# Kernel optimization log

Measured on AMD Instinct MI355X. Metric: run time of the kernel, lower is better.

The kernel has to match this reference:

```python
import jax, jax.numpy as jnp
import numpy as np

NUM_HEADS = 16
KEY_DIM = 1024
VALUE_DIM = 1024
OUTPUT_DIM = 1024
D_MODEL = 1024


def setup_inputs() -> dict:
    key = jax.random.key(0)
    ks = jax.random.split(key, 12)
    B, S = 2, 2048
    inp = {
        'V': jax.random.normal(ks[0], (B, S, D_MODEL), dtype=jnp.float32),
        'Q': jax.random.normal(ks[1], (B, S, D_MODEL), dtype=jnp.float32),
        'K': jax.random.normal(ks[2], (B, S, D_MODEL), dtype=jnp.float32),
        'mask': jnp.ones((B, S, 1), dtype=jnp.float32),
        'WQ': jax.random.normal(ks[3], (D_MODEL, KEY_DIM), dtype=jnp.float32) * (1.0 / np.sqrt(D_MODEL)),
        'bQ': jnp.zeros((KEY_DIM,), dtype=jnp.float32),
        'WK': jax.random.normal(ks[4], (D_MODEL, KEY_DIM), dtype=jnp.float32) * (1.0 / np.sqrt(D_MODEL)),
        'bK': jnp.zeros((KEY_DIM,), dtype=jnp.float32),
        'WV': jax.random.normal(ks[5], (D_MODEL, VALUE_DIM), dtype=jnp.float32) * (1.0 / np.sqrt(D_MODEL)),
        'bV': jnp.zeros((VALUE_DIM,), dtype=jnp.float32),
        'WO': jax.random.normal(ks[6], (VALUE_DIM, OUTPUT_DIM), dtype=jnp.float32) * (1.0 / np.sqrt(VALUE_DIM)),
        'bO': jnp.zeros((OUTPUT_DIM,), dtype=jnp.float32),
    }
    return inp


def _split_heads(x, H):
    # [B, S, H*Dh] -> [B, H, S, Dh]
    B, S, D = x.shape
    return x.reshape(B, S, H, D // H).transpose(0, 2, 1, 3)


def reference(V, Q, K, mask, WQ, bQ, WK, bK, WV, bV, WO, bO):
    H = NUM_HEADS
    B, S, _ = Q.shape
    q = _split_heads(Q @ WQ + bQ, H)            # [B,H,S,Dh]
    k = _split_heads(K @ WK + bK, H)            # [B,H,S,Dh]
    scores = jnp.einsum('bhqd,bhkd->bhqk', q, k) / jnp.sqrt(jnp.float32(KEY_DIM))
    # hard mask: cross_mask = mask @ mask^T, broadcast over heads
    cross = jnp.einsum('bqi,bki->bqk', mask, mask)[:, None]  # [B,1,S,S]
    scores = jnp.where(cross > 0, scores, -jnp.inf)
    w = jax.nn.softmax(scores, axis=-1)          # [B,H,S,S]
    v = _split_heads(V @ WV + bV, H)             # [B,H,S,Dh]
    ctx = jnp.einsum('bhqk,bhkd->bhqd', w, v)    # [B,H,S,Dh]
    ctx = ctx.transpose(0, 2, 1, 3).reshape(B, S, -1)  # [B,S,H*Dh]
    out = ctx @ WO + bO                          # [B,S,output_dim]
    return out * mask
```

## Files before the change

### kernel.cpp

```cpp
#include <hip/hip_runtime.h>

typedef unsigned int uint;
typedef unsigned short u16;
using bf8    = __attribute__((ext_vector_type(8))) short;
using f32x4  = __attribute__((ext_vector_type(4))) float;
using f32x16 = __attribute__((ext_vector_type(16))) float;
using u16x4  = __attribute__((ext_vector_type(4))) unsigned short;

__device__ __forceinline__ u16 f2b(float f) {
    uint u = __builtin_bit_cast(uint, f);
    u += 0x7FFFu + ((u >> 16) & 1u);
    return (u16)(u >> 16);
}

#define CVTPK(lo, hi_) ({ uint r_; asm("v_cvt_pk_bf16_f32 %0, %1, %2" : "=v"(r_) : "v"(lo), "v"(hi_)); r_; })
#define SWAP32(a, b)   asm("v_permlane32_swap_b32 %0, %1" : "+v"(a), "+v"(b))

__device__ __forceinline__ void gload16(const void* g, void* l) {
    __builtin_amdgcn_global_load_lds(
        (const __attribute__((address_space(1))) unsigned int*)g,
        (__attribute__((address_space(3))) unsigned int*)l, 16, 0, 0);
}

__device__ __forceinline__ bf8 mk_pb(float p0, float p1, float p2, float p3,
                                     float p4, float p5, float p6, float p7) {
    uint a0 = CVTPK(p0, p1), b0 = CVTPK(p4, p5);
    uint a1 = CVTPK(p2, p3), b1 = CVTPK(p6, p7);
    SWAP32(a0, b0);
    SWAP32(a1, b1);
    union { uint u[4]; bf8 v; } r;
    r.u[0] = a0; r.u[1] = a1; r.u[2] = b0; r.u[3] = b1;
    return r.v;
}

__global__ __launch_bounds__(256) void k_wt(
    const float* __restrict__ w0, const float* __restrict__ w1,
    const float* __restrict__ w2, const float* __restrict__ w3,
    u16* __restrict__ o0, u16* __restrict__ o1,
    u16* __restrict__ o2, u16* __restrict__ o3)
{
    const float* w; u16* o;
    switch (blockIdx.z) {
        case 0: w = w0; o = o0; break;
        case 1: w = w1; o = o1; break;
        case 2: w = w2; o = o2; break;
        default: w = w3; o = o3; break;
    }
    __shared__ float t[32][33];
    int n0 = blockIdx.x * 32, k0 = blockIdx.y * 32;
    int tr = threadIdx.x >> 5, tc = threadIdx.x & 31;
    for (int i = 0; i < 4; ++i) {
        int r = i * 8 + tr;
        t[r][tc] = w[(size_t)(k0 + r) * 1024 + n0 + tc];
    }
    __syncthreads();
    for (int i = 0; i < 4; ++i) {
        int r = i * 8 + tr;
        o[(size_t)(n0 + r) * 1024 + k0 + tc] = f2b(t[tc][r]);
    }
}

__global__ __launch_bounds__(256) void k_cvt(
    const float* __restrict__ s0, const float* __restrict__ s1, const float* __restrict__ s2,
    u16* __restrict__ d0, u16* __restrict__ d1, u16* __restrict__ d2)
{
    const float* s; u16* d;
    switch (blockIdx.z) {
        case 0: s = s0; d = d0; break;
        case 1: s = s1; d = d1; break;
        default: s = s2; d = d2; break;
    }
    size_t i = ((size_t)blockIdx.x * 256 + threadIdx.x) * 8;
    float4 a = *(const float4*)(s + i);
    float4 b = *(const float4*)(s + i + 4);
    uint4 o;
    o.x = CVTPK(a.x, a.y);
    o.y = CVTPK(a.z, a.w);
    o.z = CVTPK(b.x, b.y);
    o.w = CVTPK(b.z, b.w);
    *(uint4*)(d + i) = o;
}

#define GEMM_BODY(A_, Bt_)                                                          \
    __shared__ u16 lA[128 * 64];                                                    \
    __shared__ u16 lB[128 * 64];                                                    \
    int tid = threadIdx.x;                                                          \
    int lane = tid & 63, wv = tid >> 6;                                             \
    int wm = wv >> 1, wn = wv & 1;                                                  \
    int m0 = blockIdx.x * 128, n0 = blockIdx.y * 128;                               \
    int lr = lane & 15, lg = lane >> 4;                                             \
    int sRow = lane >> 3, sCol = (lane & 7) * 8;                                    \
    f32x4 acc[4][4] = {};                                                           \
    for (int k0 = 0; k0 < 1024; k0 += 64) {                                         \
        __syncthreads();                                                            \
        _Pragma("unroll")                                                           \
        for (int c = 0; c < 4; ++c) {                                               \
            int rb = c * 32 + wv * 8;                                               \
            gload16(&A_[(size_t)(m0 + rb + sRow) * 1024 + k0 + sCol],               \
                    &lA[rb * 64 + lane * 8]);                                       \
            gload16(&Bt_[(size_t)(n0 + rb + sRow) * 1024 + k0 + sCol],              \
                    &lB[rb * 64 + lane * 8]);                                       \
        }                                                                           \
        __syncthreads();                                                            \
        _Pragma("unroll")                                                           \
        for (int kk = 0; kk < 64; kk += 32) {                                       \
            bf8 af[4], bfr[4];                                                      \
            int ko = kk + lg * 8;                                                   \
            _Pragma("unroll")                                                       \
            for (int m = 0; m < 4; ++m) af[m]  = *(const bf8*)&lA[(wm * 64 + m * 16 + lr) * 64 + ko]; \
            _Pragma("unroll")                                                       \
            for (int n = 0; n < 4; ++n) bfr[n] = *(const bf8*)&lB[(wn * 64 + n * 16 + lr) * 64 + ko]; \
            _Pragma("unroll")                                                       \
            for (int m = 0; m < 4; ++m)                                             \
                _Pragma("unroll")                                                   \
                for (int n = 0; n < 4; ++n)                                         \
                    acc[m][n] = __builtin_amdgcn_mfma_f32_16x16x32_bf16(af[m], bfr[n], acc[m][n], 0, 0, 0); \
        }                                                                           \
    }

__global__ __launch_bounds__(256) void k_gemm_qkv(
    const u16* __restrict__ Xq, const u16* __restrict__ Xk, const u16* __restrict__ Xv,
    const u16* __restrict__ WtQ, const u16* __restrict__ WtK, const u16* __restrict__ WtV,
    const float* __restrict__ bQ, const float* __restrict__ bK, const float* __restrict__ bV,
    u16* __restrict__ qn, u16* __restrict__ kn, u16* __restrict__ vth, float qscale)
{
    const u16 *A, *Bt; const float* bias; u16* outp; int epi; float scale;
    switch (blockIdx.z) {
        case 0:  A = Xq; Bt = WtQ; bias = bQ; outp = qn;  epi = 0; scale = qscale; break;
        case 1:  A = Xk; Bt = WtK; bias = bK; outp = kn;  epi = 0; scale = 1.0f;   break;
        default: A = Xv; Bt = WtV; bias = bV; outp = vth; epi = 1; scale = 1.0f;   break;
    }
    GEMM_BODY(A, Bt)
    for (int m = 0; m < 4; ++m) {
        int Rb = m0 + wm * 64 + m * 16 + lg * 4;
        for (int n = 0; n < 4; ++n) {
            int C = n0 + wn * 64 + n * 16 + lr;
            float bv = bias[C];
            if (epi == 0) {
                for (int r = 0; r < 4; ++r)
                    outp[(size_t)(Rb + r) * 1024 + C] = f2b((acc[m][n][r] + bv) * scale);
            } else {
                int h = C >> 6, dh = C & 63;
                int b = Rb >> 11, s = Rb & 2047;
                u16x4 pk;
                for (int r = 0; r < 4; ++r) pk[r] = f2b(acc[m][n][r] + bv);
                *(u16x4*)&vth[((size_t)(b * 16 + h) * 64 + dh) * 2048 + s] = pk;
            }
        }
    }
}

__global__ __launch_bounds__(256) void k_gemm_out(
    const u16* __restrict__ Actx, const u16* __restrict__ WtO,
    const float* __restrict__ bias, const float* __restrict__ mask,
    float* __restrict__ outp)
{
    GEMM_BODY(Actx, WtO)
    for (int m = 0; m < 4; ++m) {
        int Rb = m0 + wm * 64 + m * 16 + lg * 4;
        for (int n = 0; n < 4; ++n) {
            int C = n0 + wn * 64 + n * 16 + lr;
            float bv = bias[C];
            for (int r = 0; r < 4; ++r) {
                int R = Rb + r;
                outp[(size_t)R * 1024 + C] = (acc[m][n][r] + bv) * mask[R];
            }
        }
    }
}

__global__ __launch_bounds__(256) void k_flash(
    const u16* __restrict__ qn, const u16* __restrict__ kn,
    const u16* __restrict__ vt, u16* __restrict__ ctx)
{
    __shared__ char lK[8192];
    __shared__ char lV[8192];
    const int S = 2048;
    int bh = blockIdx.y;
    int b = bh >> 4, h = bh & 15;
    int q0 = blockIdx.x * 128;
    int tid = threadIdx.x, lane = tid & 63, w = tid >> 6;
    int l31 = lane & 31, hi = lane >> 5;

    int qrow = q0 + w * 32 + l31;
    bf8 qf[4];
    const u16* qbase = &qn[((size_t)(b * 2048 + qrow)) * 1024 + h * 64 + hi * 8];
#pragma unroll
    for (int dk = 0; dk < 4; ++dk) qf[dk] = *(const bf8*)&qbase[dk * 16];

    bf8 ones;
#pragma unroll
    for (int i = 0; i < 8; ++i) ones[i] = (short)0x3F80;

    f32x16 o0 = {}, o1 = {}, o2 = {};

    int sr = tid >> 2;
    int sc = (tid & 3) * 32;
    const u16* gK = &kn[((size_t)(b * 2048 + sr)) * 1024 + h * 64 + (sc >> 1)];
    const u16* gV = &vt[((size_t)bh * 64 + sr) * 2048 + (sc >> 1)];
    int wA0 = sr * 128 + (sc        ^ ((sr & 7) << 4));
    int wA1 = sr * 128 + ((sc + 16) ^ ((sr & 7) << 4));

    uint4 ra0 = *(const uint4*)(gK);
    uint4 ra1 = *(const uint4*)(gK + 8);
    uint4 rb0 = *(const uint4*)(gV);
    uint4 rb1 = *(const uint4*)(gV + 8);

    int swzK = ((l31 & 7) << 4);
    for (int k0 = 0; k0 < S; k0 += 64) {
        __syncthreads();
        *(uint4*)&lK[wA0] = ra0; *(uint4*)&lK[wA1] = ra1;
        *(uint4*)&lV[wA0] = rb0; *(uint4*)&lV[wA1] = rb1;
        if (k0 + 64 < S) {
            ra0 = *(const uint4*)(gK + (size_t)(k0 + 64) * 1024);
            ra1 = *(const uint4*)(gK + (size_t)(k0 + 64) * 1024 + 8);
            rb0 = *(const uint4*)(gV + k0 + 64);
            rb1 = *(const uint4*)(gV + k0 + 64 + 8);
        }
        __syncthreads();

        f32x16 s0 = {}, s1 = {};
#pragma unroll
        for (int dk = 0; dk < 4; ++dk) {
            int cb = dk * 32 + hi * 16;
            bf8 kf0 = *(const bf8*)&lK[l31 * 128 + (cb ^ swzK)];
            bf8 kf1 = *(const bf8*)&lK[(32 + l31) * 128 + (cb ^ swzK)];
            s0 = __builtin_amdgcn_mfma_f32_32x32x16_bf16(kf0, qf[dk], s0, 0, 0, 0);
            s1 = __builtin_amdgcn_mfma_f32_32x32x16_bf16(kf1, qf[dk], s1, 0, 0, 0);
        }

#pragma unroll
        for (int i = 0; i < 16; ++i) s0[i] = __builtin_amdgcn_exp2f(s0[i]);
#pragma unroll
        for (int i = 0; i < 16; ++i) s1[i] = __builtin_amdgcn_exp2f(s1[i]);

        bf8 pb0 = mk_pb(s0[0], s0[1], s0[2],  s0[3],  s0[4],  s0[5],  s0[6],  s0[7]);
        bf8 pb1 = mk_pb(s0[8], s0[9], s0[10], s0[11], s0[12], s0[13], s0[14], s0[15]);
        bf8 pb2 = mk_pb(s1[0], s1[1], s1[2],  s1[3],  s1[4],  s1[5],  s1[6],  s1[7]);
        bf8 pb3 = mk_pb(s1[8], s1[9], s1[10], s1[11], s1[12], s1[13], s1[14], s1[15]);

#pragma unroll
        for (int ks = 0; ks < 4; ++ks) {
            bf8 pb = (ks == 0) ? pb0 : (ks == 1) ? pb1 : (ks == 2) ? pb2 : pb3;
            int cb = ks * 32 + hi * 16;
            bf8 vf0 = *(const bf8*)&lV[l31 * 128 + (cb ^ swzK)];
            bf8 vf1 = *(const bf8*)&lV[(32 + l31) * 128 + (cb ^ swzK)];
            o0 = __builtin_amdgcn_mfma_f32_32x32x16_bf16(vf0, pb, o0, 0, 0, 0);
            o1 = __builtin_amdgcn_mfma_f32_32x32x16_bf16(vf1, pb, o1, 0, 0, 0);
            o2 = __builtin_amdgcn_mfma_f32_32x32x16_bf16(ones, pb, o2, 0, 0, 0);
        }
    }

    float rinv = 1.f / o2[0];
    size_t obase = ((size_t)(b * 2048 + qrow)) * 1024 + h * 64;
#pragma unroll
    for (int k = 0; k < 4; ++k) {
        u16x4 v0, v1;
#pragma unroll
        for (int j = 0; j < 4; ++j) {
            v0[j] = f2b(o0[k * 4 + j] * rinv);
            v1[j] = f2b(o1[k * 4 + j] * rinv);
        }
        *(u16x4*)&ctx[obase + 8 * k + 4 * hi]      = v0;
        *(u16x4*)&ctx[obase + 32 + 8 * k + 4 * hi] = v1;
    }
}

extern "C" void kernel_launch(void* const* d_in, const int* in_sizes, int n_in,
                              void* d_out, int out_size, void* d_ws, size_t ws_size,
                              hipStream_t stream)
{
    const float* V    = (const float*)d_in[0];
    const float* Q    = (const float*)d_in[1];
    const float* Kin  = (const float*)d_in[2];
    const float* mask = (const float*)d_in[3];
    const float* WQ   = (const float*)d_in[4];
    const float* bQ   = (const float*)d_in[5];
    const float* WK   = (const float*)d_in[6];
    const float* bK   = (const float*)d_in[7];
    const float* WV   = (const float*)d_in[8];
    const float* bV   = (const float*)d_in[9];
    const float* WO   = (const float*)d_in[10];
    const float* bO   = (const float*)d_in[11];
    float* out = (float*)d_out;

    u16* base = (u16*)d_ws;
    const size_t NE = (size_t)4096 * 1024;
    const size_t NW = (size_t)1024 * 1024;
    u16* Xq  = base;
    u16* Xk  = Xq + NE;
    u16* Xv  = Xk + NE;
    u16* qn  = Xv + NE;
    u16* kn  = qn + NE;
    u16* vth = kn + NE;
    u16* ctx = vth + NE;
    u16* WtQ = ctx + NE;
    u16* WtK = WtQ + NW;
    u16* WtV = WtK + NW;
    u16* WtO = WtV + NW;

    const float qscale = 0.03125f * 1.44269504f;

    k_wt <<<dim3(32, 32, 4), 256, 0, stream>>>(WQ, WK, WV, WO, WtQ, WtK, WtV, WtO);
    k_cvt<<<dim3(2048, 1, 3), 256, 0, stream>>>(Q, Kin, V, Xq, Xk, Xv);
    k_gemm_qkv<<<dim3(32, 8, 3), 256, 0, stream>>>(Xq, Xk, Xv, WtQ, WtK, WtV,
                                                   bQ, bK, bV, qn, kn, vth, qscale);
    k_flash<<<dim3(16, 32), 256, 0, stream>>>(qn, kn, vth, ctx);
    k_gemm_out<<<dim3(32, 8), 256, 0, stream>>>(ctx, WtO, bO, mask, out);
}
```

Measured before the change: 142.9 us.

## Double-buffer LDS tiles in GEMM and flash attention loops

Both the projection GEMMs and the flash-attention kernel now keep two LDS buffers. The next K-tile's global-to-LDS loads are issued before computing on the current tile. The flash loop also drops from two barriers per iteration to a single hand-written waitcnt plus barrier. The aim is to hide global load latency behind MFMA work and to cut synchronisation stalls. The cost is double the LDS per block (64KB in the GEMM), which may lower occupancy.

```diff
diff --git a/kernel.cpp b/kernel.cpp
--- a/kernel.cpp
+++ b/kernel.cpp
@@ -82,8 +82,8 @@
 }
 
 #define GEMM_BODY(A_, Bt_)                                                          \
-    __shared__ u16 lA[128 * 64];                                                    \
-    __shared__ u16 lB[128 * 64];                                                    \
+    __shared__ u16 lA[2][128 * 64];                                                 \
+    __shared__ u16 lB[2][128 * 64];                                                 \
     int tid = threadIdx.x;                                                          \
     int lane = tid & 63, wv = tid >> 6;                                             \
     int wm = wv >> 1, wn = wv & 1;                                                  \
@@ -91,31 +91,41 @@
     int lr = lane & 15, lg = lane >> 4;                                             \
     int sRow = lane >> 3, sCol = (lane & 7) * 8;                                    \
     f32x4 acc[4][4] = {};                                                           \
-    for (int k0 = 0; k0 < 1024; k0 += 64) {                                         \
-        __syncthreads();                                                            \
-        _Pragma("unroll")                                                           \
-        for (int c = 0; c < 4; ++c) {                                               \
-            int rb = c * 32 + wv * 8;                                               \
-            gload16(&A_[(size_t)(m0 + rb + sRow) * 1024 + k0 + sCol],               \
-                    &lA[rb * 64 + lane * 8]);                                       \
-            gload16(&Bt_[(size_t)(n0 + rb + sRow) * 1024 + k0 + sCol],              \
-                    &lB[rb * 64 + lane * 8]);                                       \
+    _Pragma("unroll")                                                               \
+    for (int c = 0; c < 4; ++c) {                                                   \
+        int rb = c * 32 + wv * 8;                                                   \
+        gload16(&A_[(size_t)(m0 + rb + sRow) * 1024 + sCol], &lA[0][rb * 64 + lane * 8]);   \
+        gload16(&Bt_[(size_t)(n0 + rb + sRow) * 1024 + sCol], &lB[0][rb * 64 + lane * 8]);  \
+    }                                                                               \
+    __syncthreads();                                                                \
+    for (int t = 0; t < 16; ++t) {                                                  \
+        int cur = t & 1;                                                            \
+        if (t < 15) {                                                               \
+            int k1 = (t + 1) * 64;                                                  \
+            _Pragma("unroll")                                                       \
+            for (int c = 0; c < 4; ++c) {                                           \
+                int rb = c * 32 + wv * 8;                                           \
+                gload16(&A_[(size_t)(m0 + rb + sRow) * 1024 + k1 + sCol],           \
+                        &lA[cur ^ 1][rb * 64 + lane * 8]);                          \
+                gload16(&Bt_[(size_t)(n0 + rb + sRow) * 1024 + k1 + sCol],          \
+                        &lB[cur ^ 1][rb * 64 + lane * 8]);                          \
+            }                                                                       \
         }                                                                           \
-        __syncthreads();                                                            \
         _Pragma("unroll")                                                           \
         for (int kk = 0; kk < 64; kk += 32) {                                       \
             bf8 af[4], bfr[4];                                                      \
             int ko = kk + lg * 8;                                                   \
             _Pragma("unroll")                                                       \
-            for (int m = 0; m < 4; ++m) af[m]  = *(const bf8*)&lA[(wm * 64 + m * 16 + lr) * 64 + ko]; \
+            for (int m = 0; m < 4; ++m) af[m]  = *(const bf8*)&lA[cur][(wm * 64 + m * 16 + lr) * 64 + ko];  \
             _Pragma("unroll")                                                       \
-            for (int n = 0; n < 4; ++n) bfr[n] = *(const bf8*)&lB[(wn * 64 + n * 16 + lr) * 64 + ko]; \
+            for (int n = 0; n < 4; ++n) bfr[n] = *(const bf8*)&lB[cur][(wn * 64 + n * 16 + lr) * 64 + ko];  \
             _Pragma("unroll")                                                       \
             for (int m = 0; m < 4; ++m)                                             \
                 _Pragma("unroll")                                                   \
                 for (int n = 0; n < 4; ++n)                                         \
                     acc[m][n] = __builtin_amdgcn_mfma_f32_16x16x32_bf16(af[m], bfr[n], acc[m][n], 0, 0, 0); \
         }                                                                           \
+        if (t < 15) __syncthreads();                                                \
     }
 
 __global__ __launch_bounds__(256) void k_gemm_qkv(
@@ -173,8 +183,8 @@
     const u16* __restrict__ qn, const u16* __restrict__ kn,
     const u16* __restrict__ vt, u16* __restrict__ ctx)
 {
-    __shared__ char lK[8192];
-    __shared__ char lV[8192];
+    __shared__ char lK[2][8192];
+    __shared__ char lV[2][8192];
     const int S = 2048;
     int bh = blockIdx.y;
     int b = bh >> 4, h = bh & 15;
@@ -207,24 +217,25 @@
     uint4 rb1 = *(const uint4*)(gV + 8);
 
     int swzK = ((l31 & 7) << 4);
-    for (int k0 = 0; k0 < S; k0 += 64) {
-        __syncthreads();
-        *(uint4*)&lK[wA0] = ra0; *(uint4*)&lK[wA1] = ra1;
-        *(uint4*)&lV[wA0] = rb0; *(uint4*)&lV[wA1] = rb1;
-        if (k0 + 64 < S) {
-            ra0 = *(const uint4*)(gK + (size_t)(k0 + 64) * 1024);
-            ra1 = *(const uint4*)(gK + (size_t)(k0 + 64) * 1024 + 8);
-            rb0 = *(const uint4*)(gV + k0 + 64);
-            rb1 = *(const uint4*)(gV + k0 + 64 + 8);
-        }
-        __syncthreads();
+    for (int t = 0; t < 32; ++t) {
+        int cur = t & 1;
+        *(uint4*)&lK[cur][wA0] = ra0; *(uint4*)&lK[cur][wA1] = ra1;
+        *(uint4*)&lV[cur][wA0] = rb0; *(uint4*)&lV[cur][wA1] = rb1;
+        if (t < 31) {
+            int k1 = (t + 1) * 64;
+            ra0 = *(const uint4*)(gK + (size_t)k1 * 1024);
+            ra1 = *(const uint4*)(gK + (size_t)k1 * 1024 + 8);
+            rb0 = *(const uint4*)(gV + k1);
+            rb1 = *(const uint4*)(gV + k1 + 8);
+        }
+        asm volatile("s_waitcnt lgkmcnt(0)\n\ts_barrier" ::: "memory");
 
         f32x16 s0 = {}, s1 = {};
 #pragma unroll
         for (int dk = 0; dk < 4; ++dk) {
             int cb = dk * 32 + hi * 16;
-            bf8 kf0 = *(const bf8*)&lK[l31 * 128 + (cb ^ swzK)];
-            bf8 kf1 = *(const bf8*)&lK[(32 + l31) * 128 + (cb ^ swzK)];
+            bf8 kf0 = *(const bf8*)&lK[cur][l31 * 128 + (cb ^ swzK)];
+            bf8 kf1 = *(const bf8*)&lK[cur][(32 + l31) * 128 + (cb ^ swzK)];
             s0 = __builtin_amdgcn_mfma_f32_32x32x16_bf16(kf0, qf[dk], s0, 0, 0, 0);
             s1 = __builtin_amdgcn_mfma_f32_32x32x16_bf16(kf1, qf[dk], s1, 0, 0, 0);
         }
@@ -243,8 +254,8 @@
         for (int ks = 0; ks < 4; ++ks) {
             bf8 pb = (ks == 0) ? pb0 : (ks == 1) ? pb1 : (ks == 2) ? pb2 : pb3;
             int cb = ks * 32 + hi * 16;
-            bf8 vf0 = *(const bf8*)&lV[l31 * 128 + (cb ^ swzK)];
-            bf8 vf1 = *(const bf8*)&lV[(32 + l31) * 128 + (cb ^ swzK)];
+            bf8 vf0 = *(const bf8*)&lV[cur][l31 * 128 + (cb ^ swzK)];
+            bf8 vf1 = *(const bf8*)&lV[cur][(32 + l31) * 128 + (cb ^ swzK)];
             o0 = __builtin_amdgcn_mfma_f32_32x32x16_bf16(vf0, pb, o0, 0, 0, 0);
             o1 = __builtin_amdgcn_mfma_f32_32x32x16_bf16(vf1, pb, o1, 0, 0, 0);
             o2 = __builtin_amdgcn_mfma_f32_32x32x16_bf16(ones, pb, o2, 0, 0, 0);
```

Result: slower. 152.3 us (+6.6%).
